# Optimization experiments

Measured on AMD Instinct MI355X. Metric: run time of the kernel, lower is better.

Reference implementation:

```python
import jax, jax.numpy as jnp
import numpy as np

NUM_ANCHORS = 3


def _decode_scale(output, thresh, anchor, step):
    # output: [B, C, H, W] with C = 3*(5+num_classes); anchor: [3, 2]
    B, C, H, W = output.shape
    o = jnp.transpose(output, (0, 2, 3, 1)).reshape(B, H, W, NUM_ANCHORS, -1)
    conf = o[..., 0]
    mask = conf > thresh  # data-dependent filter -> expressed as dense mask (jit-safe)
    gy = jnp.arange(H, dtype=o.dtype)[None, :, None, None]  # index[:,1]
    gx = jnp.arange(W, dtype=o.dtype)[None, None, :, None]  # index[:,2]
    cx = (gx + o[..., 1]) * step
    cy = (gy + o[..., 2]) * step
    w = anchor[:, 0] * jnp.exp(o[..., 3])  # broadcast over anchor axis a
    h = anchor[:, 1] * jnp.exp(o[..., 4])
    x1 = cx - w * 0.5
    y1 = cy - h * 0.5
    x2 = x1 + w
    y2 = y1 + h
    cls = jax.lax.stop_gradient(jnp.argmax(o[..., 5:], axis=-1).astype(o.dtype))
    out = jnp.stack([conf, x1, y1, x2, y2, cls], axis=-1)  # [B,H,W,3,6]
    out = jnp.where(mask[..., None], out, jnp.zeros((), o.dtype))
    return out.reshape(-1, 6)


def setup_inputs() -> dict:
    key = jax.random.key(0)
    k13, k26, k52, ka = jax.random.split(key, 4)
    B, C = 32, 255  # 3 anchors * (5 + 80 classes)
    return {
        "output13": jax.random.normal(k13, (B, C, 13, 13), dtype=jnp.float32),
        "output26": jax.random.normal(k26, (B, C, 26, 26), dtype=jnp.float32),
        "output52": jax.random.normal(k52, (B, C, 52, 52), dtype=jnp.float32),
        "anchors": jax.random.uniform(ka, (3, 3, 2), dtype=jnp.float32),
    }


def reference(output13, output26, output52, anchors):
    out13 = _decode_scale(output13, 0.5, anchors[0], 32.0)
    out26 = _decode_scale(output26, 0.5, anchors[1], 16.0)
    out52 = _decode_scale(output52, 0.9, anchors[2], 8.0)
    return jnp.concatenate([out13, out26, out52], axis=0)
```

## Files before the change

### kernel.cpp

```cpp
#include <hip/hip_runtime.h>
#include <hip/hip_bf16.h>


#define NUM_B 32
#define NUM_CLS 80
#define CH 255

#define R13 (NUM_B * 13 * 13 * 3)
#define R26 (NUM_B * 26 * 26 * 3)
#define R52 (NUM_B * 52 * 52 * 3)
#define CUM13 R13
#define CUM26 (R13 + R26)
#define TOTAL (R13 + R26 + R52)

__global__ __launch_bounds__(256) void detector_decode(
    const float* __restrict__ in13,
    const float* __restrict__ in26,
    const float* __restrict__ in52,
    const float* __restrict__ anchors,
    float* __restrict__ out)
{
    int tid = blockIdx.x * blockDim.x + threadIdx.x;
    if (tid >= TOTAL) return;

    const float* in;
    int H;
    float thresh, step;
    int aoff;
    int r;
    if (tid < CUM13) {
        in = in13; H = 13; thresh = 0.5f; step = 32.0f; aoff = 0; r = tid;
    } else if (tid < CUM26) {
        in = in26; H = 26; thresh = 0.5f; step = 16.0f; aoff = 6; r = tid - CUM13;
    } else {
        in = in52; H = 52; thresh = 0.9f; step = 8.0f;  aoff = 12; r = tid - CUM26;
    }

    const int W  = H;
    const int HW = H * W;

    const int a    = r % 3;
    const int cell = r / 3;
    const int hw   = cell % HW;
    const int b    = cell / HW;

    const float* p = in + ((size_t)b * CH + (size_t)a * 85) * (size_t)HW + hw;

    float* o = out + (size_t)tid * 6;

    const float conf = p[0];
    if (!(conf > thresh)) {
        o[0] = 0.0f; o[1] = 0.0f; o[2] = 0.0f;
        o[3] = 0.0f; o[4] = 0.0f; o[5] = 0.0f;
        return;
    }

    const float tx = p[(size_t)1 * HW];
    const float ty = p[(size_t)2 * HW];
    const float tw = p[(size_t)3 * HW];
    const float th = p[(size_t)4 * HW];

    const int wi = hw % W;
    const int hi = hw / W;

    const float cx = ((float)wi + tx) * step;
    const float cy = ((float)hi + ty) * step;
    const float aw = anchors[aoff + a * 2 + 0] * __expf(tw) ;
    const float ah = anchors[aoff + a * 2 + 1] * __expf(th) ;

    const float x1 = cx - aw * 0.5f;
    const float y1 = cy - ah * 0.5f;
    const float x2 = x1 + aw;
    const float y2 = y1 + ah;

    const float* pc = p + (size_t)5 * HW;
    float best = pc[0];
    int bi = 0;
    #pragma unroll 8
    for (int c = 1; c < NUM_CLS; ++c) {
        float v = pc[(size_t)c * HW];
        if (v > best) { best = v; bi = c; }
    }

    o[0] = conf;
    o[1] = x1;
    o[2] = y1;
    o[3] = x2;
    o[4] = y2;
    o[5] = (float)bi;
}

extern "C" void kernel_launch(void* const* d_in, const int* in_sizes, int n_in,
                              void* d_out, int out_size, void* d_ws, size_t ws_size,
                              hipStream_t stream) {
    const float* in13    = (const float*)d_in[0];
    const float* in26    = (const float*)d_in[1];
    const float* in52    = (const float*)d_in[2];
    const float* anchors = (const float*)d_in[3];
    float* out = (float*)d_out;

    const int threads = 256;
    const int blocks  = (TOTAL + threads - 1) / threads;
    detector_decode<<<blocks, threads, 0, stream>>>(in13, in26, in52, anchors, out);
}
```

Baseline: 32.65 us.

## Template decode per scale, batch class loads, remove early-exit branch

```diff
diff --git a/kernel.cpp b/kernel.cpp
--- a/kernel.cpp
+++ b/kernel.cpp
@@ -13,6 +13,64 @@
 #define CUM26 (R13 + R26)
 #define TOTAL (R13 + R26 + R52)
 
+template <int H, int AOFF>
+__device__ __forceinline__ void decode_row(
+    const float* __restrict__ in,
+    const float* __restrict__ anchors,
+    float thresh, float step,
+    int r,
+    float* __restrict__ orow)
+{
+    constexpr int W  = H;
+    constexpr int HW = H * W;
+
+    const int a    = r % 3;
+    const int cell = r / 3;
+    const int hw   = cell % HW;
+    const int b    = cell / HW;
+
+    const float* p = in + ((size_t)(b * CH + a * 85)) * HW + hw;
+
+    const float conf = p[0];
+    const float tx   = p[1 * HW];
+    const float ty   = p[2 * HW];
+    const float tw   = p[3 * HW];
+    const float th   = p[4 * HW];
+
+    const float* pc = p + 5 * HW;
+    float best = -3.402823466e+38f;
+    int   bi   = 0;
+    #pragma unroll
+    for (int c0 = 0; c0 < NUM_CLS; c0 += 16) {
+        float v[16];
+        #pragma unroll
+        for (int k = 0; k < 16; ++k)
+            v[k] = pc[(size_t)(c0 + k) * HW];
+        #pragma unroll
+        for (int k = 0; k < 16; ++k)
+            if (v[k] > best) { best = v[k]; bi = c0 + k; }
+    }
+
+    const int wi = hw % W;
+    const int hi = hw / W;
+
+    const float cx = ((float)wi + tx) * step;
+    const float cy = ((float)hi + ty) * step;
+    const float aw = anchors[AOFF + a * 2 + 0] * __expf(tw);
+    const float ah = anchors[AOFF + a * 2 + 1] * __expf(th);
+
+    const float x1 = cx - aw * 0.5f;
+    const float y1 = cy - ah * 0.5f;
+    const float x2 = x1 + aw;
+    const float y2 = y1 + ah;
+
+    const bool m = conf > thresh;
+    float2* o2 = (float2*)orow;
+    o2[0] = m ? make_float2(conf, x1)       : make_float2(0.f, 0.f);
+    o2[1] = m ? make_float2(y1, x2)         : make_float2(0.f, 0.f);
+    o2[2] = m ? make_float2(y2, (float)bi)  : make_float2(0.f, 0.f);
+}
+
 __global__ __launch_bounds__(256) void detector_decode(
     const float* __restrict__ in13,
     const float* __restrict__ in26,
@@ -23,71 +81,15 @@
     int tid = blockIdx.x * blockDim.x + threadIdx.x;
     if (tid >= TOTAL) return;
 
-    const float* in;
-    int H;
-    float thresh, step;
-    int aoff;
-    int r;
+    float* orow = out + (size_t)tid * 6;
+
     if (tid < CUM13) {
-        in = in13; H = 13; thresh = 0.5f; step = 32.0f; aoff = 0; r = tid;
+        decode_row<13, 0>(in13, anchors, 0.5f, 32.0f, tid, orow);
     } else if (tid < CUM26) {
-        in = in26; H = 26; thresh = 0.5f; step = 16.0f; aoff = 6; r = tid - CUM13;
+        decode_row<26, 6>(in26, anchors, 0.5f, 16.0f, tid - CUM13, orow);
     } else {
-        in = in52; H = 52; thresh = 0.9f; step = 8.0f;  aoff = 12; r = tid - CUM26;
+        decode_row<52, 12>(in52, anchors, 0.9f, 8.0f, tid - CUM26, orow);
     }
-
-    const int W  = H;
-    const int HW = H * W;
-
-    const int a    = r % 3;
-    const int cell = r / 3;
-    const int hw   = cell % HW;
-    const int b    = cell / HW;
-
-    const float* p = in + ((size_t)b * CH + (size_t)a * 85) * (size_t)HW + hw;
-
-    float* o = out + (size_t)tid * 6;
-
-    const float conf = p[0];
-    if (!(conf > thresh)) {
-        o[0] = 0.0f; o[1] = 0.0f; o[2] = 0.0f;
-        o[3] = 0.0f; o[4] = 0.0f; o[5] = 0.0f;
-        return;
-    }
-
-    const float tx = p[(size_t)1 * HW];
-    const float ty = p[(size_t)2 * HW];
-    const float tw = p[(size_t)3 * HW];
-    const float th = p[(size_t)4 * HW];
-
-    const int wi = hw % W;
-    const int hi = hw / W;
-
-    const float cx = ((float)wi + tx) * step;
-    const float cy = ((float)hi + ty) * step;
-    const float aw = anchors[aoff + a * 2 + 0] * __expf(tw) ;
-    const float ah = anchors[aoff + a * 2 + 1] * __expf(th) ;
-
-    const float x1 = cx - aw * 0.5f;
-    const float y1 = cy - ah * 0.5f;
-    const float x2 = x1 + aw;
-    const float y2 = y1 + ah;
-
-    const float* pc = p + (size_t)5 * HW;
-    float best = pc[0];
-    int bi = 0;
-    #pragma unroll 8
-    for (int c = 1; c < NUM_CLS; ++c) {
-        float v = pc[(size_t)c * HW];
-        if (v > best) { best = v; bi = c; }
-    }
-
-    o[0] = conf;
-    o[1] = x1;
-    o[2] = y1;
-    o[3] = x2;
-    o[4] = y2;
-    o[5] = (float)bi;
 }
 
 extern "C" void kernel_launch(void* const* d_in, const int* in_sizes, int n_in,
```

Result: slower. 37.00 us (+13.3%).
